# Kernel tuning notes

Hardware: AMD Instinct MI355X
Metric: run time of the kernel (lower is better)

Reference implementation:

```python
import jax, jax.numpy as jnp
import numpy as np

N_NODES = 50000
N_EDGES = 800000
IN_F = 256
OUT_F = 128
ALPHA = 0.2  # LeakyReLU negative slope


def setup_inputs() -> dict:
    key = jax.random.key(0)
    k_h, k_row, k_col, k_W, k_a = jax.random.split(key, 5)
    h = jax.random.normal(k_h, (N_NODES, IN_F), dtype=jnp.float32)
    row = jax.random.randint(k_row, (N_EDGES,), 0, N_NODES)
    # Guarantee every node appears as a destination so unique(dst) == arange(N)
    col = jnp.concatenate([
        jnp.arange(N_NODES),
        jax.random.randint(k_col, (N_EDGES - N_NODES,), 0, N_NODES),
    ])
    adj = jnp.stack([row, col]).astype(jnp.int64)
    # Xavier-uniform-ish params (gain 1.414)
    lim_W = 1.414 * np.sqrt(6.0 / (IN_F + OUT_F))
    W = jax.random.uniform(k_W, (IN_F, OUT_F), minval=-lim_W, maxval=lim_W, dtype=jnp.float32)
    lim_a = 1.414 * np.sqrt(6.0 / (2 * OUT_F + 1))
    a = jax.random.uniform(k_a, (2 * OUT_F, 1), minval=-lim_a, maxval=lim_a, dtype=jnp.float32)
    return {"h": h, "adj": adj, "W": W, "a": a}


def reference(h, adj, W, a):
    N = h.shape[0]
    self_loops = jnp.arange(N)  # == unique(adj[1]) by input construction
    row = jnp.concatenate([adj[0], self_loops])  # [E_total]
    col = jnp.concatenate([adj[1], self_loops])  # [E_total]

    Wh = h @ W                                    # [N, OUT_F]
    s_src = (Wh @ a[:OUT_F]).squeeze(-1)          # [N] (Wh1)
    s_dst = (Wh @ a[OUT_F:]).squeeze(-1)          # [N] (Wh2)

    e = jax.nn.leaky_relu(s_dst[col] + s_src[row], negative_slope=ALPHA)  # [E_total]

    # segment softmax over destination nodes
    e_max = jax.ops.segment_max(e, col, num_segments=N)
    ex = jnp.exp(e - e_max[col])
    denom = jax.ops.segment_sum(ex, col, num_segments=N)
    att = ex / denom[col]                         # [E_total]

    h_prime = jax.ops.segment_sum(Wh[row] * att[:, None], col, num_segments=N)  # [N, OUT_F]
    return jax.nn.elu(h_prime)  # concat=True
```

## Files before the change

### kernel.cpp

```cpp
#include <hip/hip_runtime.h>
#include <math.h>

#define N_NODES 50000
#define N_EDGES 800000
#define IN_F 256
#define OUT_F 128
#define ALPHA 0.2f
#define SLOT_CAP 64
#define CNT_STRIDE 16

#define NODE_BLOCKS ((N_NODES + 255) / 256)
#define GEMM_WAVES ((N_NODES + 15) / 16)
#define GEMM_BLOCKS ((GEMM_WAVES + 3) / 4)
#define EDGE_BLOCKS ((N_EDGES + 255) / 256)

typedef short bf16x8 __attribute__((ext_vector_type(8)));
typedef float f32x4  __attribute__((ext_vector_type(4)));

static __device__ __forceinline__ unsigned short f2bf(float f) {
    unsigned int u = __float_as_uint(f);
    u += 0x7FFFu + ((u >> 16) & 1u);
    return (unsigned short)(u >> 16);
}
static __device__ __forceinline__ float bf2f(unsigned int u16) {
    return __uint_as_float(u16 << 16);
}

__global__ __launch_bounds__(256) void k_prep(const float* __restrict__ W,
                                              const float* __restrict__ a,
                                              int* __restrict__ cnt,
                                              float* __restrict__ Wa,
                                              unsigned short* __restrict__ WbT) {
    const int b = blockIdx.x, t = threadIdx.x;
    if (b < NODE_BLOCKS) {
        int i = b * 256 + t;
        if (i < N_NODES) {
            int4 z = make_int4(0, 0, 0, 0);
            int4* p = (int4*)(cnt + (size_t)i * CNT_STRIDE);
            p[0] = z; p[1] = z; p[2] = z; p[3] = z;
        }
    } else if (b == NODE_BLOCKS) {
        const int k = t;
        const float4* wr  = (const float4*)(W + (size_t)k * OUT_F);
        const float4* av1 = (const float4*)a;
        const float4* av2 = (const float4*)(a + OUT_F);
        float s1 = 0.0f, s2 = 0.0f;
#pragma unroll 8
        for (int i = 0; i < OUT_F / 4; ++i) {
            float4 w = wr[i], x = av1[i], y = av2[i];
            s1 = fmaf(w.x, x.x, fmaf(w.y, x.y, fmaf(w.z, x.z, fmaf(w.w, x.w, s1))));
            s2 = fmaf(w.x, y.x, fmaf(w.y, y.y, fmaf(w.z, y.z, fmaf(w.w, y.w, s2))));
        }
        Wa[k] = s1;
        Wa[IN_F + k] = s2;
    } else {
        const int n = b - (NODE_BLOCKS + 1);
        WbT[(size_t)n * IN_F + t] = f2bf(W[(size_t)t * OUT_F + n]);
    }
}

__global__ __launch_bounds__(256) void k_main(const float* __restrict__ h,
                                              const unsigned short* __restrict__ WbT,
                                              const float* __restrict__ Wa,
                                              const int* __restrict__ adj,
                                              unsigned short* __restrict__ Whb,
                                              float* __restrict__ s_src,
                                              float* __restrict__ s_dst,
                                              int* __restrict__ cnt,
                                              int* __restrict__ slots) {
    if (blockIdx.x >= GEMM_BLOCKS) {
        const int e = (blockIdx.x - GEMM_BLOCKS) * 256 + threadIdx.x;
        if (e < N_EDGES) {
            const int src = adj[e];
            const int dst = adj[N_EDGES + e];
            const int p = atomicAdd(&cnt[(size_t)dst * CNT_STRIDE], 1);
            if (p < SLOT_CAP) slots[(size_t)dst * SLOT_CAP + p] = src;
        }
        return;
    }
    const int wid = blockIdx.x * 4 + (threadIdx.x >> 6);
    if (wid >= GEMM_WAVES) return;
    const int lane = threadIdx.x & 63;
    const int m = lane & 15, grp = lane >> 4;
    const int row = wid * 16 + m;

    f32x4 acc[8];
#pragma unroll
    for (int nt = 0; nt < 8; ++nt) acc[nt] = (f32x4){0.f, 0.f, 0.f, 0.f};
    float sp1 = 0.0f, sp2 = 0.0f;

    const float* hrow = h + (size_t)row * IN_F;
    for (int kt = 0; kt < 8; ++kt) {
        const int k0 = kt * 32 + grp * 8;
        const float4* hp = (const float4*)(hrow + k0);
        float4 x0 = hp[0], x1 = hp[1];
        const float4* wap1 = (const float4*)(Wa + k0);
        const float4* wap2 = (const float4*)(Wa + IN_F + k0);
        float4 a0 = wap1[0], a1 = wap1[1];
        float4 b0 = wap2[0], b1 = wap2[1];
        sp1 = fmaf(x0.x, a0.x, fmaf(x0.y, a0.y, fmaf(x0.z, a0.z, fmaf(x0.w, a0.w, sp1))));
        sp1 = fmaf(x1.x, a1.x, fmaf(x1.y, a1.y, fmaf(x1.z, a1.z, fmaf(x1.w, a1.w, sp1))));
        sp2 = fmaf(x0.x, b0.x, fmaf(x0.y, b0.y, fmaf(x0.z, b0.z, fmaf(x0.w, b0.w, sp2))));
        sp2 = fmaf(x1.x, b1.x, fmaf(x1.y, b1.y, fmaf(x1.z, b1.z, fmaf(x1.w, b1.w, sp2))));
        bf16x8 hf;
        hf[0] = (short)f2bf(x0.x); hf[1] = (short)f2bf(x0.y);
        hf[2] = (short)f2bf(x0.z); hf[3] = (short)f2bf(x0.w);
        hf[4] = (short)f2bf(x1.x); hf[5] = (short)f2bf(x1.y);
        hf[6] = (short)f2bf(x1.z); hf[7] = (short)f2bf(x1.w);
#pragma unroll
        for (int nt = 0; nt < 8; ++nt) {
            bf16x8 wf = *(const bf16x8*)(WbT + (size_t)(nt * 16 + m) * IN_F + k0);
            acc[nt] = __builtin_amdgcn_mfma_f32_16x16x32_bf16(wf, hf, acc[nt], 0, 0, 0);
        }
    }

    float t1 = sp1, t2 = sp2;
    t1 += __shfl_xor(t1, 16); t1 += __shfl_xor(t1, 32);
    t2 += __shfl_xor(t2, 16); t2 += __shfl_xor(t2, 32);
    if (grp == 0) { s_src[row] = t1; s_dst[row] = t2; }

    unsigned short* orow = Whb + (size_t)row * OUT_F;
#pragma unroll
    for (int nt = 0; nt < 8; ++nt) {
        f32x4 v = acc[nt];
        ushort4 pk;
        pk.x = f2bf(v[0]); pk.y = f2bf(v[1]);
        pk.z = f2bf(v[2]); pk.w = f2bf(v[3]);
        *(ushort4*)(orow + nt * 16 + grp * 4) = pk;
    }
}

__global__ __launch_bounds__(256) void k_gather(const unsigned short* __restrict__ Whb,
                                                const int* __restrict__ cnt,
                                                const int* __restrict__ slots,
                                                const float* __restrict__ s_src,
                                                const float* __restrict__ s_dst,
                                                float* __restrict__ out) {
    const int wid  = (blockIdx.x * blockDim.x + threadIdx.x) >> 6;
    const int lane = threadIdx.x & 63;
    const int grp  = lane >> 4;
    const int l    = lane & 15;
    const int node = wid * 4 + grp;
    if (node >= N_NODES) return;

    const float sd = s_dst[node];
    float s0 = sd + s_src[node];
    float lr0 = (s0 > 0.0f) ? s0 : ALPHA * s0;
    float x0 = __expf(lr0);
    uint4 w0 = ((const uint4*)(Whb + (size_t)node * OUT_F))[l];
    float a0 = x0 * bf2f(w0.x & 0xFFFFu);
    float a1 = x0 * bf2f(w0.x >> 16);
    float a2 = x0 * bf2f(w0.y & 0xFFFFu);
    float a3 = x0 * bf2f(w0.y >> 16);
    float a4 = x0 * bf2f(w0.z & 0xFFFFu);
    float a5 = x0 * bf2f(w0.z >> 16);
    float a6 = x0 * bf2f(w0.w & 0xFFFFu);
    float a7 = x0 * bf2f(w0.w >> 16);
    float dsum = x0;

    const int deg = min(cnt[(size_t)node * CNT_STRIDE], SLOT_CAP);
    const int* __restrict__ srow = slots + (size_t)node * SLOT_CAP;

    for (int i = 0; i < deg; i += 4) {
        const int4 q = *(const int4*)(srow + i);
        const unsigned su0 = min((unsigned)q.x, N_NODES - 1u);
        const unsigned su1 = min((unsigned)q.y, N_NODES - 1u);
        const unsigned su2 = min((unsigned)q.z, N_NODES - 1u);
        const unsigned su3 = min((unsigned)q.w, N_NODES - 1u);
        const float e0 = sd + s_src[su0];
        const float e1 = sd + s_src[su1];
        const float e2 = sd + s_src[su2];
        const float e3 = sd + s_src[su3];
        const uint4 v0 = ((const uint4*)(Whb + (size_t)su0 * OUT_F))[l];
        const uint4 v1 = ((const uint4*)(Whb + (size_t)su1 * OUT_F))[l];
        const uint4 v2 = ((const uint4*)(Whb + (size_t)su2 * OUT_F))[l];
        const uint4 v3 = ((const uint4*)(Whb + (size_t)su3 * OUT_F))[l];
        float x_0 = __expf((e0 > 0.0f) ? e0 : ALPHA * e0);
        float x_1 = __expf((e1 > 0.0f) ? e1 : ALPHA * e1);
        float x_2 = __expf((e2 > 0.0f) ? e2 : ALPHA * e2);
        float x_3 = __expf((e3 > 0.0f) ? e3 : ALPHA * e3);
        x_1 = (i + 1 < deg) ? x_1 : 0.0f;
        x_2 = (i + 2 < deg) ? x_2 : 0.0f;
        x_3 = (i + 3 < deg) ? x_3 : 0.0f;
        dsum += x_0 + x_1 + x_2 + x_3;
        a0 = fmaf(x_0, bf2f(v0.x & 0xFFFFu), a0);
        a1 = fmaf(x_0, bf2f(v0.x >> 16), a1);
        a2 = fmaf(x_0, bf2f(v0.y & 0xFFFFu), a2);
        a3 = fmaf(x_0, bf2f(v0.y >> 16), a3);
        a4 = fmaf(x_0, bf2f(v0.z & 0xFFFFu), a4);
        a5 = fmaf(x_0, bf2f(v0.z >> 16), a5);
        a6 = fmaf(x_0, bf2f(v0.w & 0xFFFFu), a6);
        a7 = fmaf(x_0, bf2f(v0.w >> 16), a7);
        a0 = fmaf(x_1, bf2f(v1.x & 0xFFFFu), a0);
        a1 = fmaf(x_1, bf2f(v1.x >> 16), a1);
        a2 = fmaf(x_1, bf2f(v1.y & 0xFFFFu), a2);
        a3 = fmaf(x_1, bf2f(v1.y >> 16), a3);
        a4 = fmaf(x_1, bf2f(v1.z & 0xFFFFu), a4);
        a5 = fmaf(x_1, bf2f(v1.z >> 16), a5);
        a6 = fmaf(x_1, bf2f(v1.w & 0xFFFFu), a6);
        a7 = fmaf(x_1, bf2f(v1.w >> 16), a7);
        a0 = fmaf(x_2, bf2f(v2.x & 0xFFFFu), a0);
        a1 = fmaf(x_2, bf2f(v2.x >> 16), a1);
        a2 = fmaf(x_2, bf2f(v2.y & 0xFFFFu), a2);
        a3 = fmaf(x_2, bf2f(v2.y >> 16), a3);
        a4 = fmaf(x_2, bf2f(v2.z & 0xFFFFu), a4);
        a5 = fmaf(x_2, bf2f(v2.z >> 16), a5);
        a6 = fmaf(x_2, bf2f(v2.w & 0xFFFFu), a6);
        a7 = fmaf(x_2, bf2f(v2.w >> 16), a7);
        a0 = fmaf(x_3, bf2f(v3.x & 0xFFFFu), a0);
        a1 = fmaf(x_3, bf2f(v3.x >> 16), a1);
        a2 = fmaf(x_3, bf2f(v3.y & 0xFFFFu), a2);
        a3 = fmaf(x_3, bf2f(v3.y >> 16), a3);
        a4 = fmaf(x_3, bf2f(v3.z & 0xFFFFu), a4);
        a5 = fmaf(x_3, bf2f(v3.z >> 16), a5);
        a6 = fmaf(x_3, bf2f(v3.w & 0xFFFFu), a6);
        a7 = fmaf(x_3, bf2f(v3.w >> 16), a7);
    }

    const float inv = 1.0f / dsum;
    float4 o0, o1;
    o0.x = a0 * inv; o0.y = a1 * inv; o0.z = a2 * inv; o0.w = a3 * inv;
    o1.x = a4 * inv; o1.y = a5 * inv; o1.z = a6 * inv; o1.w = a7 * inv;
    o0.x = (o0.x > 0.0f) ? o0.x : expm1f(o0.x);
    o0.y = (o0.y > 0.0f) ? o0.y : expm1f(o0.y);
    o0.z = (o0.z > 0.0f) ? o0.z : expm1f(o0.z);
    o0.w = (o0.w > 0.0f) ? o0.w : expm1f(o0.w);
    o1.x = (o1.x > 0.0f) ? o1.x : expm1f(o1.x);
    o1.y = (o1.y > 0.0f) ? o1.y : expm1f(o1.y);
    o1.z = (o1.z > 0.0f) ? o1.z : expm1f(o1.z);
    o1.w = (o1.w > 0.0f) ? o1.w : expm1f(o1.w);
    float4* op = (float4*)(out + (size_t)node * OUT_F + l * 8);
    op[0] = o0;
    op[1] = o1;
}

extern "C" void kernel_launch(void* const* d_in, const int* in_sizes, int n_in,
                              void* d_out, int out_size, void* d_ws, size_t ws_size,
                              hipStream_t stream) {
    const float* h   = (const float*)d_in[0];
    const int*   adj = (const int*)d_in[1];
    const float* W   = (const float*)d_in[2];
    const float* a   = (const float*)d_in[3];
    float* out = (float*)d_out;

    char* ws = (char*)d_ws;
    const size_t SZ_WHB = (size_t)N_NODES * OUT_F * 2;
    const size_t SZ_N   = 200704;
    const size_t SZ_CNT = (size_t)N_NODES * CNT_STRIDE * 4;
    unsigned short* Whb = (unsigned short*)(ws);
    float* s_src   = (float*)(ws + SZ_WHB);
    float* s_dst   = (float*)(ws + SZ_WHB + SZ_N);
    int*   cnt     = (int*)  (ws + SZ_WHB + 2 * SZ_N);
    float* Wa      = (float*)(ws + SZ_WHB + 2 * SZ_N + SZ_CNT);
    unsigned short* WbT = (unsigned short*)(ws + SZ_WHB + 2 * SZ_N + SZ_CNT + 2048);
    int*   slots   = (int*)  (ws + SZ_WHB + 2 * SZ_N + SZ_CNT + 2048 + 65536);

    (void)in_sizes; (void)n_in; (void)out_size; (void)ws_size;

    k_prep  <<<NODE_BLOCKS + 1 + OUT_F, 256, 0, stream>>>(W, a, cnt, Wa, WbT);
    k_main  <<<GEMM_BLOCKS + EDGE_BLOCKS, 256, 0, stream>>>(h, WbT, Wa, adj, Whb,
                                                            s_src, s_dst, cnt, slots);
    k_gather<<<(N_NODES / 4 * 64) / 256, 256, 0, stream>>>(Whb, cnt, slots,
                                                           s_src, s_dst, out);
}
```

Measured before the change: 197.2 us.

## Split scatter into its own vectorized kernel and halve GEMM output per wave

The edge-scatter work moves out of the fused GEMM kernel into a separate kernel that handles four edges per thread using int4 loads of src and dst. The GEMM kernel now assigns two waves to each 16-row tile, each computing 64 of the 128 output columns, which doubles wave-level parallelism and halves accumulator registers. Only the first half computes the attention score dot products, and the k loop is fully unrolled. The cost is that each h row is loaded twice, an extra kernel launch is added, and scatter no longer runs concurrently with the GEMM inside one launch.

```diff
diff --git a/kernel.cpp b/kernel.cpp
--- a/kernel.cpp
+++ b/kernel.cpp
@@ -10,9 +10,10 @@
 #define CNT_STRIDE 16
 
 #define NODE_BLOCKS ((N_NODES + 255) / 256)
-#define GEMM_WAVES ((N_NODES + 15) / 16)
+#define GEMM_WAVES (2 * ((N_NODES + 15) / 16))
 #define GEMM_BLOCKS ((GEMM_WAVES + 3) / 4)
-#define EDGE_BLOCKS ((N_EDGES + 255) / 256)
+#define SCAT_THREADS (N_EDGES / 4)
+#define SCAT_BLOCKS ((SCAT_THREADS + 255) / 256)
 
 typedef short bf16x8 __attribute__((ext_vector_type(8)));
 typedef float f32x4  __attribute__((ext_vector_type(4)));
@@ -59,69 +60,80 @@
     }
 }
 
-__global__ __launch_bounds__(256) void k_main(const float* __restrict__ h,
+__global__ __launch_bounds__(256) void k_scatter(const int* __restrict__ adj,
+                                                 int* __restrict__ cnt,
+                                                 int* __restrict__ slots) {
+    const int t = blockIdx.x * 256 + threadIdx.x;
+    if (t >= SCAT_THREADS) return;
+    const int4 s4 = ((const int4*)adj)[t];
+    const int4 d4 = ((const int4*)(adj + N_EDGES))[t];
+    const int p0 = atomicAdd(&cnt[(size_t)d4.x * CNT_STRIDE], 1);
+    const int p1 = atomicAdd(&cnt[(size_t)d4.y * CNT_STRIDE], 1);
+    const int p2 = atomicAdd(&cnt[(size_t)d4.z * CNT_STRIDE], 1);
+    const int p3 = atomicAdd(&cnt[(size_t)d4.w * CNT_STRIDE], 1);
+    if (p0 < SLOT_CAP) slots[(size_t)d4.x * SLOT_CAP + p0] = s4.x;
+    if (p1 < SLOT_CAP) slots[(size_t)d4.y * SLOT_CAP + p1] = s4.y;
+    if (p2 < SLOT_CAP) slots[(size_t)d4.z * SLOT_CAP + p2] = s4.z;
+    if (p3 < SLOT_CAP) slots[(size_t)d4.w * SLOT_CAP + p3] = s4.w;
+}
+
+__global__ __launch_bounds__(256) void k_gemm(const float* __restrict__ h,
                                               const unsigned short* __restrict__ WbT,
                                               const float* __restrict__ Wa,
-                                              const int* __restrict__ adj,
                                               unsigned short* __restrict__ Whb,
                                               float* __restrict__ s_src,
-                                              float* __restrict__ s_dst,
-                                              int* __restrict__ cnt,
-                                              int* __restrict__ slots) {
-    if (blockIdx.x >= GEMM_BLOCKS) {
-        const int e = (blockIdx.x - GEMM_BLOCKS) * 256 + threadIdx.x;
-        if (e < N_EDGES) {
-            const int src = adj[e];
-            const int dst = adj[N_EDGES + e];
-            const int p = atomicAdd(&cnt[(size_t)dst * CNT_STRIDE], 1);
-            if (p < SLOT_CAP) slots[(size_t)dst * SLOT_CAP + p] = src;
-        }
-        return;
-    }
+                                              float* __restrict__ s_dst) {
     const int wid = blockIdx.x * 4 + (threadIdx.x >> 6);
     if (wid >= GEMM_WAVES) return;
     const int lane = threadIdx.x & 63;
     const int m = lane & 15, grp = lane >> 4;
-    const int row = wid * 16 + m;
-
-    f32x4 acc[8];
-#pragma unroll
-    for (int nt = 0; nt < 8; ++nt) acc[nt] = (f32x4){0.f, 0.f, 0.f, 0.f};
+    const int row  = (wid >> 1) * 16 + m;
+    const int half = wid & 1;
+    const unsigned short* wbase = WbT + (size_t)(half * 64 + m) * IN_F + grp * 8;
+    const float* hrow = h + (size_t)row * IN_F + grp * 8;
+
+    f32x4 acc[4];
+#pragma unroll
+    for (int nt = 0; nt < 4; ++nt) acc[nt] = (f32x4){0.f, 0.f, 0.f, 0.f};
     float sp1 = 0.0f, sp2 = 0.0f;
 
-    const float* hrow = h + (size_t)row * IN_F;
+#pragma unroll
     for (int kt = 0; kt < 8; ++kt) {
-        const int k0 = kt * 32 + grp * 8;
+        const int k0 = kt * 32;
         const float4* hp = (const float4*)(hrow + k0);
         float4 x0 = hp[0], x1 = hp[1];
-        const float4* wap1 = (const float4*)(Wa + k0);
-        const float4* wap2 = (const float4*)(Wa + IN_F + k0);
-        float4 a0 = wap1[0], a1 = wap1[1];
-        float4 b0 = wap2[0], b1 = wap2[1];
-        sp1 = fmaf(x0.x, a0.x, fmaf(x0.y, a0.y, fmaf(x0.z, a0.z, fmaf(x0.w, a0.w, sp1))));
-        sp1 = fmaf(x1.x, a1.x, fmaf(x1.y, a1.y, fmaf(x1.z, a1.z, fmaf(x1.w, a1.w, sp1))));
-        sp2 = fmaf(x0.x, b0.x, fmaf(x0.y, b0.y, fmaf(x0.z, b0.z, fmaf(x0.w, b0.w, sp2))));
-        sp2 = fmaf(x1.x, b1.x, fmaf(x1.y, b1.y, fmaf(x1.z, b1.z, fmaf(x1.w, b1.w, sp2))));
+        if (half == 0) {
+            const float4* wap1 = (const float4*)(Wa + k0 + grp * 8);
+            const float4* wap2 = (const float4*)(Wa + IN_F + k0 + grp * 8);
+            float4 a0 = wap1[0], a1 = wap1[1];
+            float4 b0 = wap2[0], b1 = wap2[1];
+            sp1 = fmaf(x0.x, a0.x, fmaf(x0.y, a0.y, fmaf(x0.z, a0.z, fmaf(x0.w, a0.w, sp1))));
+            sp1 = fmaf(x1.x, a1.x, fmaf(x1.y, a1.y, fmaf(x1.z, a1.z, fmaf(x1.w, a1.w, sp1))));
+            sp2 = fmaf(x0.x, b0.x, fmaf(x0.y, b0.y, fmaf(x0.z, b0.z, fmaf(x0.w, b0.w, sp2))));
+            sp2 = fmaf(x1.x, b1.x, fmaf(x1.y, b1.y, fmaf(x1.z, b1.z, fmaf(x1.w, b1.w, sp2))));
+        }
         bf16x8 hf;
         hf[0] = (short)f2bf(x0.x); hf[1] = (short)f2bf(x0.y);
         hf[2] = (short)f2bf(x0.z); hf[3] = (short)f2bf(x0.w);
         hf[4] = (short)f2bf(x1.x); hf[5] = (short)f2bf(x1.y);
         hf[6] = (short)f2bf(x1.z); hf[7] = (short)f2bf(x1.w);
 #pragma unroll
-        for (int nt = 0; nt < 8; ++nt) {
-            bf16x8 wf = *(const bf16x8*)(WbT + (size_t)(nt * 16 + m) * IN_F + k0);
+        for (int nt = 0; nt < 4; ++nt) {
+            bf16x8 wf = *(const bf16x8*)(wbase + (size_t)nt * 16 * IN_F + k0);
             acc[nt] = __builtin_amdgcn_mfma_f32_16x16x32_bf16(wf, hf, acc[nt], 0, 0, 0);
         }
     }
 
-    float t1 = sp1, t2 = sp2;
-    t1 += __shfl_xor(t1, 16); t1 += __shfl_xor(t1, 32);
-    t2 += __shfl_xor(t2, 16); t2 += __shfl_xor(t2, 32);
-    if (grp == 0) { s_src[row] = t1; s_dst[row] = t2; }
-
-    unsigned short* orow = Whb + (size_t)row * OUT_F;
-#pragma unroll
-    for (int nt = 0; nt < 8; ++nt) {
+    if (half == 0) {
+        float t1 = sp1, t2 = sp2;
+        t1 += __shfl_xor(t1, 16); t1 += __shfl_xor(t1, 32);
+        t2 += __shfl_xor(t2, 16); t2 += __shfl_xor(t2, 32);
+        if (grp == 0) { s_src[row] = t1; s_dst[row] = t2; }
+    }
+
+    unsigned short* orow = Whb + (size_t)row * OUT_F + half * 64;
+#pragma unroll
+    for (int nt = 0; nt < 4; ++nt) {
         f32x4 v = acc[nt];
         ushort4 pk;
         pk.x = f2bf(v[0]); pk.y = f2bf(v[1]);
@@ -257,9 +269,9 @@
 
     (void)in_sizes; (void)n_in; (void)out_size; (void)ws_size;
 
-    k_prep  <<<NODE_BLOCKS + 1 + OUT_F, 256, 0, stream>>>(W, a, cnt, Wa, WbT);
-    k_main  <<<GEMM_BLOCKS + EDGE_BLOCKS, 256, 0, stream>>>(h, WbT, Wa, adj, Whb,
-                                                            s_src, s_dst, cnt, slots);
-    k_gather<<<(N_NODES / 4 * 64) / 256, 256, 0, stream>>>(Whb, cnt, slots,
-                                                           s_src, s_dst, out);
-}
+    k_prep   <<<NODE_BLOCKS + 1 + OUT_F, 256, 0, stream>>>(W, a, cnt, Wa, WbT);
+    k_scatter<<<SCAT_BLOCKS, 256, 0, stream>>>(adj, cnt, slots);
+    k_gemm   <<<GEMM_BLOCKS, 256, 0, stream>>>(h, WbT, Wa, Whb, s_src, s_dst);
+    k_gather <<<(N_NODES / 4 * 64) / 256, 256, 0, stream>>>(Whb, cnt, slots,
+                                                            s_src, s_dst, out);
+}
```

New measurement: 216.6 us. 1.1x slower.
